# Performance work log

Measured on AMD Instinct MI355X. Metric: run time of the kernel, lower is better.

The kernel has to match this reference:

```python
import jax, jax.numpy as jnp
import numpy as np

B, N_VIS, N_TXT = 2, 2048, 256
N_HEAD, HEAD_DIM = 16, 64
C = N_HEAD * HEAD_DIM  # 1024
EPS = 1e-6


def setup_inputs() -> dict:
    key = jax.random.key(0)
    ks = jax.random.split(key, 24)
    s = 0.02
    inp = {
        'vis_x': jax.random.normal(ks[0], (B, N_VIS, C), jnp.float32),
        'txt_x': jax.random.normal(ks[1], (B, N_TXT, C), jnp.float32),
        'rope_cos': jax.random.uniform(ks[2], (N_VIS, HEAD_DIM), jnp.float32, -1.0, 1.0),
        'rope_sin': jax.random.uniform(ks[3], (N_VIS, HEAD_DIM), jnp.float32, -1.0, 1.0),
    }
    names = ['vis_qw', 'vis_kw', 'vis_vw', 'vis_ow', 'txt_qw', 'txt_kw', 'txt_vw', 'txt_ow']
    for i, n in enumerate(names):
        inp[n] = jax.random.normal(ks[4 + i], (C, C), jnp.float32) * s
        inp[n[:-1] + 'b'] = jnp.zeros((C,), jnp.float32)
    for n in ['vis_qn', 'vis_kn', 'txt_qn', 'txt_kn']:
        inp[n] = jnp.ones((HEAD_DIM,), jnp.float32)
    return inp


def _heads(x, w, b):
    # x: [B,N,C] -> [B,H,N,D]  (torch Linear: x @ W.T + b)
    y = x @ w.T + b
    Bn, N, _ = y.shape
    return y.reshape(Bn, N, N_HEAD, HEAD_DIM).transpose(0, 2, 1, 3)


def _rmsnorm(x, g):
    return x * jax.lax.rsqrt(jnp.mean(x * x, axis=-1, keepdims=True) + EPS) * g


def _rope(x, cos, sin):
    # interleaved-pair rotation: pairs (x0,x1) -> (-x1, x0)
    xr, xi = x[..., 0::2], x[..., 1::2]
    rot = jnp.stack([-xi, xr], axis=-1).reshape(x.shape)
    return x * cos[None, None] + rot * sin[None, None]


def reference(vis_x, txt_x, rope_cos, rope_sin,
              vis_qw, vis_qb, vis_kw, vis_kb, vis_vw, vis_vb, vis_ow, vis_ob,
              txt_qw, txt_qb, txt_kw, txt_kb, txt_vw, txt_vb, txt_ow, txt_ob,
              vis_qn, vis_kn, txt_qn, txt_kn):
    q_vis = _rmsnorm(_heads(vis_x, vis_qw, vis_qb), vis_qn)
    k_vis = _rmsnorm(_heads(vis_x, vis_kw, vis_kb), vis_kn)
    v_vis = _heads(vis_x, vis_vw, vis_vb)
    q_txt = _rmsnorm(_heads(txt_x, txt_qw, txt_qb), txt_qn)
    k_txt = _rmsnorm(_heads(txt_x, txt_kw, txt_kb), txt_kn)
    v_txt = _heads(txt_x, txt_vw, txt_vb)

    q_vis = _rope(q_vis, rope_cos, rope_sin)
    k_vis = _rope(k_vis, rope_cos, rope_sin)

    q = jnp.concatenate([q_txt, q_vis], axis=2)  # [B,H,S,D]
    k = jnp.concatenate([k_txt, k_vis], axis=2)
    v = jnp.concatenate([v_txt, v_vis], axis=2)

    scale = 1.0 / jnp.sqrt(jnp.asarray(HEAD_DIM, q.dtype))
    scores = jnp.einsum('bhqd,bhkd->bhqk', q, k) * scale
    attn = jax.nn.softmax(scores, axis=-1)
    out = jnp.einsum('bhqk,bhkd->bhqd', attn, v)  # [B,H,S,D]

    txt_out = out[:, :, :N_TXT, :].transpose(0, 2, 1, 3).reshape(q.shape[0], N_TXT, C)
    vis_out = out[:, :, N_TXT:, :].transpose(0, 2, 1, 3).reshape(q.shape[0], N_VIS, C)
    vis_out = vis_out @ vis_ow.T + vis_ob
    txt_out = txt_out @ txt_ow.T + txt_ob
    return (vis_out, txt_out)
```

## Files before the change

### kernel.cpp

```cpp
#include <hip/hip_runtime.h>

typedef _Float16 h8 __attribute__((ext_vector_type(8)));
typedef _Float16 h4 __attribute__((ext_vector_type(4)));
typedef _Float16 h2 __attribute__((ext_vector_type(2)));
typedef float f4 __attribute__((ext_vector_type(4)));
typedef float f16x16 __attribute__((ext_vector_type(16)));

#define LOG2E 1.44269504088896340736f

__device__ __forceinline__ void gload_lds16(const void* g, void* l) {
    __builtin_amdgcn_global_load_lds(
        (const __attribute__((address_space(1))) void*)g,
        (__attribute__((address_space(3))) void*)l, 16, 0, 0);
}

struct CastArgs { const float* src[10]; _Float16* dst[10]; };

__global__ __launch_bounds__(256) void cast_all_kernel(CastArgs a) {
    int blk = blockIdx.x;
    int seg, rel;
    if (blk < 4096)      { seg = 0; rel = blk; }
    else if (blk < 4608) { seg = 1; rel = blk - 4096; }
    else { int t = blk - 4608; seg = 2 + (t >> 10); rel = t & 1023; }
    long base = ((long)rel * 256 + threadIdx.x) * 4;
    float4 v = *(const float4*)(a.src[seg] + base);
    h4 o = { (_Float16)v.x, (_Float16)v.y, (_Float16)v.z, (_Float16)v.w };
    *(h4*)(a.dst[seg] + base) = o;
}

struct GemmDesc {
    const _Float16* A[2];
    const _Float16* W[2];
    char*           C[2];
    const float*    bias[2][3];
    long bsA[2];
    long aoff[2];
    long bsC[2];
    int  mshift[2];
    int  mcut;
};

template<bool OUT_F32>
__global__ __launch_bounds__(256)
void gemm_kernel(GemmDesc g, int K, int N, int gm, int gn, int xgn)
{
    __shared__ __align__(16) _Float16 As[128 * 64];
    __shared__ __align__(16) _Float16 Bs[128 * 64];
    const int lane = threadIdx.x & 63;
    const int wave = threadIdx.x >> 6;
    const int lid = blockIdx.x;
    const int xcd = lid & 7;
    const int r0 = lid >> 3;
    const int mtile = (xcd / xgn) * gm + (r0 % gm);
    const int ntile = (xcd % xgn) * gn + (r0 / gm);

    const int seg = mtile >= g.mcut;
    const int mloc = mtile - (seg ? g.mcut : 0);
    const int bidx = mloc >> g.mshift[seg];
    const int min_ = mloc & ((1 << g.mshift[seg]) - 1);
    const _Float16* Ab = g.A[seg] + (long)bidx * g.bsA[seg] + g.aoff[seg]
                         + (long)min_ * 128 * K;
    const _Float16* Bb = g.W[seg] + (long)ntile * 128 * K;
    const long crow0 = (long)bidx * g.bsC[seg] + (long)min_ * 128 * N;

    const int wr = wave >> 1, wc = wave & 1;
    f4 acc[4][4] = {};

    for (int kt = 0; kt < K; kt += 64) {
        __syncthreads();
#pragma unroll
        for (int it = 0; it < 4; ++it) {
            int r = wave * 32 + it * 8 + (lane >> 3);
            int lc = (lane & 7) ^ (r & 7);
            gload_lds16((const char*)(Ab + (long)r * K + kt) + lc * 16,
                        (char*)As + (wave * 32 + it * 8) * 128);
            gload_lds16((const char*)(Bb + (long)r * K + kt) + lc * 16,
                        (char*)Bs + (wave * 32 + it * 8) * 128);
        }
        asm volatile("s_waitcnt vmcnt(0)" ::: "memory");
        __syncthreads();
#pragma unroll
        for (int kk = 0; kk < 2; ++kk) {
            h8 af[4], bf[4];
#pragma unroll
            for (int m = 0; m < 4; ++m) {
                int row = wr * 64 + m * 16 + (lane & 15);
                int pc = (kk * 4 + (lane >> 4)) ^ (row & 7);
                af[m] = *(const h8*)(&As[row * 64 + pc * 8]);
            }
#pragma unroll
            for (int n = 0; n < 4; ++n) {
                int row = wc * 64 + n * 16 + (lane & 15);
                int pc = (kk * 4 + (lane >> 4)) ^ (row & 7);
                bf[n] = *(const h8*)(&Bs[row * 64 + pc * 8]);
            }
#pragma unroll
            for (int m = 0; m < 4; ++m)
#pragma unroll
                for (int n = 0; n < 4; ++n)
                    acc[m][n] = __builtin_amdgcn_mfma_f32_16x16x32_f16(
                        af[m], bf[n], acc[m][n], 0, 0, 0);
        }
    }

#pragma unroll
    for (int n = 0; n < 4; ++n) {
        int col = ntile * 128 + wc * 64 + n * 16 + (lane & 15);
        const float* bp = (col < 1024) ? g.bias[seg][0]
                        : (col < 2048) ? g.bias[seg][1] : g.bias[seg][2];
        float bv = bp[col & 1023];
#pragma unroll
        for (int m = 0; m < 4; ++m) {
            int lrow = wr * 64 + m * 16 + ((lane >> 4) << 2);
#pragma unroll
            for (int r = 0; r < 4; ++r) {
                float v = acc[m][n][r] + bv;
                long off = crow0 + (long)(lrow + r) * N + col;
                if (OUT_F32) ((float*)g.C[seg])[off] = v;
                else         ((_Float16*)g.C[seg])[off] = (_Float16)v;
            }
        }
    }
}

__device__ __forceinline__ float ssum8(h8 v) {
    float s = 0.f;
#pragma unroll
    for (int j = 0; j < 8; ++j) { float f = (float)v[j]; s += f * f; }
    return s;
}
__device__ __forceinline__ float red8(float s) {
    s += __shfl_xor(s, 1); s += __shfl_xor(s, 2); s += __shfl_xor(s, 4);
    return s;
}
__device__ __forceinline__ h8 norm_rope(h8 v, float rs_, const float* g, float gmul,
                                        const float* cs, const float* sn, int vis) {
    float f[8];
#pragma unroll
    for (int j = 0; j < 8; ++j) f[j] = (float)v[j] * rs_ * g[j] * gmul;
    h8 o;
    if (vis) {
#pragma unroll
        for (int j = 0; j < 8; j += 2) {
            float a = f[j], b = f[j + 1];
            o[j]     = (_Float16)(a * cs[j]     - b * sn[j]);
            o[j + 1] = (_Float16)(b * cs[j + 1] + a * sn[j + 1]);
        }
    } else {
#pragma unroll
        for (int j = 0; j < 8; ++j) o[j] = (_Float16)f[j];
    }
    return o;
}

__global__ __launch_bounds__(256)
void pass2_kernel(const _Float16* __restrict__ Yv, const _Float16* __restrict__ Yt,
                  const float* __restrict__ gqv, const float* __restrict__ gkv_,
                  const float* __restrict__ gqt, const float* __restrict__ gkt,
                  const float* __restrict__ rc, const float* __restrict__ rs,
                  _Float16* __restrict__ Q, _Float16* __restrict__ Kd,
                  _Float16* __restrict__ Vt)
{
    const int wave = threadIdx.x >> 6;
    const int lane = threadIdx.x & 63;
    const int row = blockIdx.x * 4 + wave;
    const int is_vis = row < 4096;
    const _Float16* y;
    const float *gq, *gk;
    int b, n, npos;
    if (is_vis) {
        y = Yv + (long)row * 3072; gq = gqv; gk = gkv_;
        b = row >> 11; n = row & 2047; npos = 256 + n;
    } else {
        int r2 = row - 4096;
        y = Yt + (long)r2 * 3072; gq = gqt; gk = gkt;
        b = r2 >> 8; n = r2 & 255; npos = n;
    }
    const int h0 = lane >> 3;
    const int d0 = (lane & 7) * 8;

    h8 q0 = *(const h8*)(y + lane * 8);
    h8 q1 = *(const h8*)(y + 512 + lane * 8);
    h8 k0 = *(const h8*)(y + 1024 + lane * 8);
    h8 k1 = *(const h8*)(y + 1536 + lane * 8);
    h8 v0 = *(const h8*)(y + 2048 + lane * 8);
    h8 v1 = *(const h8*)(y + 2560 + lane * 8);

    float ga[8], gb[8];
    *(float4*)(ga)     = *(const float4*)(gq + d0);
    *(float4*)(ga + 4) = *(const float4*)(gq + d0 + 4);
    *(float4*)(gb)     = *(const float4*)(gk + d0);
    *(float4*)(gb + 4) = *(const float4*)(gk + d0 + 4);
    float cs[8], sn[8];
    if (is_vis) {
        *(float4*)(cs)     = *(const float4*)(rc + n * 64 + d0);
        *(float4*)(cs + 4) = *(const float4*)(rc + n * 64 + d0 + 4);
        *(float4*)(sn)     = *(const float4*)(rs + n * 64 + d0);
        *(float4*)(sn + 4) = *(const float4*)(rs + n * 64 + d0 + 4);
    }

    const float rq0 = rsqrtf(red8(ssum8(q0)) * (1.0f / 64.0f) + 1e-6f);
    const float rq1 = rsqrtf(red8(ssum8(q1)) * (1.0f / 64.0f) + 1e-6f);
    const float rk0 = rsqrtf(red8(ssum8(k0)) * (1.0f / 64.0f) + 1e-6f);
    const float rk1 = rsqrtf(red8(ssum8(k1)) * (1.0f / 64.0f) + 1e-6f);

    const float qmul = 0.125f * LOG2E;
    const long obA = (((long)b * 16 + h0)      * 2304 + npos) * 64 + d0;
    const long obB = (((long)b * 16 + h0 + 8)  * 2304 + npos) * 64 + d0;
    *(h8*)(Q + obA)  = norm_rope(q0, rq0, ga, qmul, cs, sn, is_vis);
    *(h8*)(Q + obB)  = norm_rope(q1, rq1, ga, qmul, cs, sn, is_vis);
    *(h8*)(Kd + obA) = norm_rope(k0, rk0, gb, 1.0f, cs, sn, is_vis);
    *(h8*)(Kd + obB) = norm_rope(k1, rk1, gb, 1.0f, cs, sn, is_vis);

    const long vbA = ((long)(b * 16 + h0)     * 64 + d0) * 2304 + npos;
    const long vbB = ((long)(b * 16 + h0 + 8) * 64 + d0) * 2304 + npos;
#pragma unroll
    for (int j = 0; j < 8; ++j) {
        Vt[vbA + (long)j * 2304] = v0[j];
        Vt[vbB + (long)j * 2304] = v1[j];
    }
}

__device__ __forceinline__ void attn_stage(const char* Kt, const char* Vt, char* S,
                                           int bufB, int t,
                                           int gK0, int gK1, int gV0, int gV1,
                                           int ldsW) {
    const char* kt = Kt + (long)t * 8192;
    const char* vt = Vt + (long)t * 128;
    gload_lds16(kt + gK0, S + bufB + ldsW);
    gload_lds16(kt + gK1, S + bufB + 4096 + ldsW);
    gload_lds16(vt + gV0, S + 16384 + bufB + ldsW);
    gload_lds16(vt + gV1, S + 16384 + bufB + 4096 + ldsW);
}

__device__ __forceinline__ void pv_half(const float* p, const char* S, int vbase,
                                        const int* off, int kblk,
                                        f16x16* oacc, float& psum) {
    const h2 one2 = {(_Float16)1.f, (_Float16)1.f};
#pragma unroll
    for (int kb = 0; kb < 2; ++kb) {
        unsigned w0 = __builtin_bit_cast(unsigned,
            __builtin_amdgcn_cvt_pkrtz(p[8 * kb + 0], p[8 * kb + 1]));
        unsigned w1 = __builtin_bit_cast(unsigned,
            __builtin_amdgcn_cvt_pkrtz(p[8 * kb + 2], p[8 * kb + 3]));
        unsigned w2 = __builtin_bit_cast(unsigned,
            __builtin_amdgcn_cvt_pkrtz(p[8 * kb + 4], p[8 * kb + 5]));
        unsigned w3 = __builtin_bit_cast(unsigned,
            __builtin_amdgcn_cvt_pkrtz(p[8 * kb + 6], p[8 * kb + 7]));
        psum = __builtin_amdgcn_fdot2(__builtin_bit_cast(h2, w0), one2, psum, false);
        psum = __builtin_amdgcn_fdot2(__builtin_bit_cast(h2, w1), one2, psum, false);
        psum = __builtin_amdgcn_fdot2(__builtin_bit_cast(h2, w2), one2, psum, false);
        psum = __builtin_amdgcn_fdot2(__builtin_bit_cast(h2, w3), one2, psum, false);
        asm("v_permlane32_swap_b32 %0, %1" : "+v"(w0), "+v"(w2));
        asm("v_permlane32_swap_b32 %0, %1" : "+v"(w1), "+v"(w3));
        union { unsigned u[4]; h8 v; } pa;
        pa.u[0] = w0; pa.u[1] = w1; pa.u[2] = w2; pa.u[3] = w3;
#pragma unroll
        for (int dblk = 0; dblk < 2; ++dblk) {
            h8 vb = *(const h8*)(S + vbase + dblk * 4096 + off[kblk * 2 + kb]);
            oacc[dblk] = __builtin_amdgcn_mfma_f32_32x32x16_f16(
                pa.v, vb, oacc[dblk], 0, 0, 0);
        }
    }
}

__device__ __forceinline__ void attn_tile(const char* S, int bufB, const int* off,
                                          const h8* qf, f16x16* oacc, float& psum) {
    const f16x16 kZero = {};
    f16x16 st0, st1;
    {
        h8 ka0 = *(const h8*)(S + bufB + off[0]);
        h8 ka1 = *(const h8*)(S + bufB + 4096 + off[0]);
        st0 = __builtin_amdgcn_mfma_f32_32x32x16_f16(ka0, qf[0], kZero, 0, 0, 0);
        st1 = __builtin_amdgcn_mfma_f32_32x32x16_f16(ka1, qf[0], kZero, 0, 0, 0);
    }
#pragma unroll
    for (int ds = 1; ds < 4; ++ds) {
        h8 ka0 = *(const h8*)(S + bufB + off[ds]);
        h8 ka1 = *(const h8*)(S + bufB + 4096 + off[ds]);
        st0 = __builtin_amdgcn_mfma_f32_32x32x16_f16(ka0, qf[ds], st0, 0, 0, 0);
        st1 = __builtin_amdgcn_mfma_f32_32x32x16_f16(ka1, qf[ds], st1, 0, 0, 0);
    }
    float p0[16], p1[16];
#pragma unroll
    for (int r = 0; r < 16; ++r) { p0[r] = exp2f(st0[r]); p1[r] = exp2f(st1[r]); }
    pv_half(p0, S, 16384 + bufB, off, 0, oacc, psum);
    pv_half(p1, S, 16384 + bufB, off, 1, oacc, psum);
}

__global__ __launch_bounds__(256, 4)
void attn_kernel(const _Float16* __restrict__ Qg,
                 const _Float16* __restrict__ Kg,
                 const _Float16* __restrict__ Vg,
                 _Float16* __restrict__ Op,
                 float* __restrict__ Lp,
                 int nt, int cpx)
{
    __shared__ __align__(16) char S[32768];
    const int lane = threadIdx.x & 63;
    const int wave = threadIdx.x >> 6;
    const int l31 = lane & 31, hi = lane >> 5;
    const int d0 = blockIdx.x;
    const int id = (d0 & 7) * cpx + (d0 >> 3);
    const int split = id / 576;
    const int rem = id - split * 576;
    const int bh = rem / 18;
    const int qb = rem - bh * 18;
    const int b = bh >> 4, h = bh & 15;
    const _Float16* Qbh = Qg + (long)bh * 2304 * 64;
    const char* Kt = (const char*)(Kg + (long)bh * 2304 * 64) + (long)split * nt * 8192;
    const char* Vt = (const char*)(Vg + (long)bh * 64 * 2304) + (long)split * nt * 128;
    _Float16* Ops = Op + (long)split * 4718592;
    float* Lps = Lp + (long)split * 73728;
    const int q0 = qb * 128 + wave * 32;

    h8 qf[4];
#pragma unroll
    for (int ds = 0; ds < 4; ++ds)
        qf[ds] = *(const h8*)(Qbh + (long)(q0 + l31) * 64 + ds * 16 + hi * 8);

    const int sg16 = ((lane & 7) ^ (lane >> 3)) * 16;
    const int rK = wave * 8 + (lane >> 3);
    const int gK0 = rK * 128 + sg16;
    const int gK1 = gK0 + 32 * 128;
    const int gV0 = rK * 4608 + sg16;
    const int gV1 = gV0 + 32 * 4608;
    const int ldsW = wave * 1024;
    int off[4];
#pragma unroll
    for (int j = 0; j < 4; ++j)
        off[j] = l31 * 128 + (((j * 2 + hi) ^ (l31 & 7)) * 16);

    f16x16 oacc[2] = {};
    float psum = 0.f;

    attn_stage(Kt, Vt, S, 0, 0, gK0, gK1, gV0, gV1, ldsW);
    asm volatile("s_waitcnt vmcnt(0)" ::: "memory");
    __syncthreads();

    int t = 0;
#pragma unroll 1
    for (int pr = 0; pr < (nt - 1) >> 1; ++pr) {
        attn_stage(Kt, Vt, S, 8192, t + 1, gK0, gK1, gV0, gV1, ldsW);
        __builtin_amdgcn_s_setprio(1);
        attn_tile(S, 0, off, qf, oacc, psum);
        __builtin_amdgcn_s_setprio(0);
        asm volatile("s_waitcnt vmcnt(0)" ::: "memory");
        __syncthreads();
        attn_stage(Kt, Vt, S, 0, t + 2, gK0, gK1, gV0, gV1, ldsW);
        __builtin_amdgcn_s_setprio(1);
        attn_tile(S, 8192, off, qf, oacc, psum);
        __builtin_amdgcn_s_setprio(0);
        asm volatile("s_waitcnt vmcnt(0)" ::: "memory");
        __syncthreads();
        t += 2;
    }
    if (nt & 1) {
        __builtin_amdgcn_s_setprio(1);
        attn_tile(S, 0, off, qf, oacc, psum);
        __builtin_amdgcn_s_setprio(0);
    } else {
        attn_stage(Kt, Vt, S, 8192, nt - 1, gK0, gK1, gV0, gV1, ldsW);
        __builtin_amdgcn_s_setprio(1);
        attn_tile(S, 0, off, qf, oacc, psum);
        __builtin_amdgcn_s_setprio(0);
        asm volatile("s_waitcnt vmcnt(0)" ::: "memory");
        __syncthreads();
        __builtin_amdgcn_s_setprio(1);
        attn_tile(S, 8192, off, qf, oacc, psum);
        __builtin_amdgcn_s_setprio(0);
    }

    float lsum = psum + __shfl_xor(psum, 32);
    if (hi == 0) Lps[(long)bh * 2304 + q0 + l31] = lsum;
#pragma unroll
    for (int dblk = 0; dblk < 2; ++dblk) {
        int dcol = h * 64 + dblk * 32 + l31;
#pragma unroll
        for (int r = 0; r < 16; ++r) {
            int qrow = q0 + (r & 3) + 8 * (r >> 2) + 4 * hi;
            Ops[((long)b * 2304 + qrow) * 1024 + dcol] = (_Float16)oacc[dblk][r];
        }
    }
}

__global__ __launch_bounds__(256)
void combine_kernel(const _Float16* __restrict__ Op,
                    const float* __restrict__ Lp,
                    _Float16* __restrict__ Oh, int ns)
{
    long i = ((long)blockIdx.x * 256 + threadIdx.x) * 8;
    long row = i >> 10;
    int bb = row >= 2304;
    int n = (int)row - bb * 2304;
    int h = ((int)i & 1023) >> 6;
    long lidx = ((long)(bb * 16 + h)) * 2304 + n;
    float l = 0.f;
    float acc[8] = {};
    for (int s = 0; s < ns; ++s) {
        l += Lp[(long)s * 73728 + lidx];
        h8 a = *(const h8*)(Op + (long)s * 4718592 + i);
#pragma unroll
        for (int j = 0; j < 8; ++j) acc[j] += (float)a[j];
    }
    float inv = 1.0f / l;
    h8 o;
#pragma unroll
    for (int j = 0; j < 8; ++j) o[j] = (_Float16)(acc[j] * inv);
    *(h8*)(Oh + i) = o;
}

extern "C" void kernel_launch(void* const* d_in, const int* in_sizes, int n_in,
                              void* d_out, int out_size, void* d_ws, size_t ws_size,
                              hipStream_t stream)
{
    const float* vis_x    = (const float*)d_in[0];
    const float* txt_x    = (const float*)d_in[1];
    const float* rope_cos = (const float*)d_in[2];
    const float* rope_sin = (const float*)d_in[3];
    const float* vis_qw = (const float*)d_in[4];
    const float* vis_qb = (const float*)d_in[5];
    const float* vis_kw = (const float*)d_in[6];
    const float* vis_kb = (const float*)d_in[7];
    const float* vis_vw = (const float*)d_in[8];
    const float* vis_vb = (const float*)d_in[9];
    const float* vis_ow = (const float*)d_in[10];
    const float* vis_ob = (const float*)d_in[11];
    const float* txt_qw = (const float*)d_in[12];
    const float* txt_qb = (const float*)d_in[13];
    const float* txt_kw = (const float*)d_in[14];
    const float* txt_kb = (const float*)d_in[15];
    const float* txt_vw = (const float*)d_in[16];
    const float* txt_vb = (const float*)d_in[17];
    const float* txt_ow = (const float*)d_in[18];
    const float* txt_ob = (const float*)d_in[19];
    const float* vis_qn = (const float*)d_in[20];
    const float* vis_kn = (const float*)d_in[21];
    const float* txt_qn = (const float*)d_in[22];
    const float* txt_kn = (const float*)d_in[23];

    char* ws = (char*)d_ws;
    _Float16* Xvis  = (_Float16*)(ws);
    _Float16* Xtxt  = (_Float16*)(ws + 8388608);
    _Float16* Qh    = (_Float16*)(ws);
    _Float16* WqkvV = (_Float16*)(ws + 9437184);
    _Float16* WqkvT = (_Float16*)(ws + 15728640);
    _Float16* WoV   = (_Float16*)(ws + 22020096);
    _Float16* WoT   = (_Float16*)(ws + 24117248);
    _Float16* Yvis  = (_Float16*)(ws + 26214400);
    _Float16* Ytxt  = (_Float16*)(ws + 51380224);
    _Float16* Kh    = (_Float16*)(ws + 54525952);
    _Float16* Vth   = (_Float16*)(ws + 63963136);

    const int ns = (ws_size >= 112328704) ? 4 : 2;
    const int nt = (ns == 4) ? 9 : 18;
    _Float16* OpP;
    if (ns == 4) OpP = (_Float16*)(ws + 73400320);
    else         OpP = (_Float16*)(ws + 26214400);
    float* LpP = (float*)((char*)OpP + (size_t)ns * 9437184);
    _Float16* Oh = OpP;

    CastArgs ca;
    ca.src[0] = vis_x;  ca.dst[0] = Xvis;
    ca.src[1] = txt_x;  ca.dst[1] = Xtxt;
    ca.src[2] = vis_qw; ca.dst[2] = WqkvV;
    ca.src[3] = vis_kw; ca.dst[3] = WqkvV + 1048576;
    ca.src[4] = vis_vw; ca.dst[4] = WqkvV + 2097152;
    ca.src[5] = txt_qw; ca.dst[5] = WqkvT;
    ca.src[6] = txt_kw; ca.dst[6] = WqkvT + 1048576;
    ca.src[7] = txt_vw; ca.dst[7] = WqkvT + 2097152;
    ca.src[8] = vis_ow; ca.dst[8] = WoV;
    ca.src[9] = txt_ow; ca.dst[9] = WoT;
    cast_all_kernel<<<12800, 256, 0, stream>>>(ca);

    GemmDesc gq;
    gq.A[0] = Xvis;  gq.A[1] = Xtxt;
    gq.W[0] = WqkvV; gq.W[1] = WqkvT;
    gq.C[0] = (char*)Yvis; gq.C[1] = (char*)Ytxt;
    gq.bias[0][0] = vis_qb; gq.bias[0][1] = vis_kb; gq.bias[0][2] = vis_vb;
    gq.bias[1][0] = txt_qb; gq.bias[1][1] = txt_kb; gq.bias[1][2] = txt_vb;
    gq.bsA[0] = 0; gq.bsA[1] = 0;
    gq.aoff[0] = 0; gq.aoff[1] = 0;
    gq.bsC[0] = 0; gq.bsC[1] = 0;
    gq.mshift[0] = 5; gq.mshift[1] = 5;
    gq.mcut = 32;
    gemm_kernel<false><<<864, 256, 0, stream>>>(gq, 1024, 3072, 9, 12, 2);

    pass2_kernel<<<1152, 256, 0, stream>>>(
        Yvis, Ytxt, vis_qn, vis_kn, txt_qn, txt_kn, rope_cos, rope_sin,
        Qh, Kh, Vth);

    attn_kernel<<<576 * ns, 256, 0, stream>>>(Qh, Kh, Vth, OpP, LpP, nt, 72 * ns);
    combine_kernel<<<2304, 256, 0, stream>>>(OpP, LpP, Oh, ns);

    GemmDesc go;
    go.A[0] = Oh; go.A[1] = Oh;
    go.W[0] = WoV; go.W[1] = WoT;
    go.C[0] = (char*)d_out; go.C[1] = (char*)((float*)d_out + 4194304);
    go.bias[0][0] = vis_ob; go.bias[0][1] = vis_ob; go.bias[0][2] = vis_ob;
    go.bias[1][0] = txt_ob; go.bias[1][1] = txt_ob; go.bias[1][2] = txt_ob;
    go.bsA[0] = 2359296;  go.bsA[1] = 2359296;
    go.aoff[0] = 262144;  go.aoff[1] = 0;
    go.bsC[0] = 2097152;  go.bsC[1] = 262144;
    go.mshift[0] = 4; go.mshift[1] = 1;
    go.mcut = 32;
    gemm_kernel<true><<<288, 256, 0, stream>>>(go, 1024, 1024, 9, 4, 2);
}
```

Before: 196.0 us.

## Double-buffer GEMM LDS tiles and restructure attention loop with partial vmcnt waits

The GEMM kernel moves from a single LDS buffer to two, so it prefetches the next K tile with global_load_lds while computing on the current one. It waits with vmcnt(8) so only the older tile's loads have to complete. The attention loop is rewritten as a single ping-pong loop that also waits on only the older stage (vmcnt(4)) and uses raw s_barrier macros in place of __syncthreads. This is meant to overlap global loads with MFMA work and cut barrier stalls, at the cost of twice the GEMM LDS (64KB), which may lower occupancy.

```diff
diff --git a/kernel.cpp b/kernel.cpp
--- a/kernel.cpp
+++ b/kernel.cpp
@@ -7,6 +7,11 @@
 typedef float f16x16 __attribute__((ext_vector_type(16)));
 
 #define LOG2E 1.44269504088896340736f
+
+#define BARRIER_ACQ do { __builtin_amdgcn_s_barrier(); \
+                         asm volatile("" ::: "memory"); } while (0)
+#define BARRIER_REL do { asm volatile("" ::: "memory"); \
+                         __builtin_amdgcn_s_barrier(); } while (0)
 
 __device__ __forceinline__ void gload_lds16(const void* g, void* l) {
     __builtin_amdgcn_global_load_lds(
@@ -44,8 +49,8 @@
 __global__ __launch_bounds__(256)
 void gemm_kernel(GemmDesc g, int K, int N, int gm, int gn, int xgn)
 {
-    __shared__ __align__(16) _Float16 As[128 * 64];
-    __shared__ __align__(16) _Float16 Bs[128 * 64];
+    __shared__ __align__(16) _Float16 As[2][128 * 64];
+    __shared__ __align__(16) _Float16 Bs[2][128 * 64];
     const int lane = threadIdx.x & 63;
     const int wave = threadIdx.x >> 6;
     const int lid = blockIdx.x;
@@ -66,41 +71,54 @@
     const int wr = wave >> 1, wc = wave & 1;
     f4 acc[4][4] = {};
 
-    for (int kt = 0; kt < K; kt += 64) {
-        __syncthreads();
+    auto stage = [&](int bf, int kt) {
 #pragma unroll
         for (int it = 0; it < 4; ++it) {
             int r = wave * 32 + it * 8 + (lane >> 3);
             int lc = (lane & 7) ^ (r & 7);
             gload_lds16((const char*)(Ab + (long)r * K + kt) + lc * 16,
-                        (char*)As + (wave * 32 + it * 8) * 128);
+                        (char*)&As[bf][0] + (wave * 32 + it * 8) * 128);
             gload_lds16((const char*)(Bb + (long)r * K + kt) + lc * 16,
-                        (char*)Bs + (wave * 32 + it * 8) * 128);
-        }
-        asm volatile("s_waitcnt vmcnt(0)" ::: "memory");
-        __syncthreads();
+                        (char*)&Bs[bf][0] + (wave * 32 + it * 8) * 128);
+        }
+    };
+
+    const int nk = K >> 6;
+    stage(0, 0);
+    int buf = 0;
+#pragma unroll 1
+    for (int ki = 0; ki < nk; ++ki) {
+        if (ki + 1 < nk) {
+            stage(buf ^ 1, (ki + 1) << 6);
+            asm volatile("s_waitcnt vmcnt(8)" ::: "memory");
+        } else {
+            asm volatile("s_waitcnt vmcnt(0)" ::: "memory");
+        }
+        BARRIER_ACQ;
 #pragma unroll
         for (int kk = 0; kk < 2; ++kk) {
-            h8 af[4], bf[4];
+            h8 af[4], bf4[4];
 #pragma unroll
             for (int m = 0; m < 4; ++m) {
                 int row = wr * 64 + m * 16 + (lane & 15);
                 int pc = (kk * 4 + (lane >> 4)) ^ (row & 7);
-                af[m] = *(const h8*)(&As[row * 64 + pc * 8]);
+                af[m] = *(const h8*)(&As[buf][row * 64 + pc * 8]);
             }
 #pragma unroll
             for (int n = 0; n < 4; ++n) {
                 int row = wc * 64 + n * 16 + (lane & 15);
                 int pc = (kk * 4 + (lane >> 4)) ^ (row & 7);
-                bf[n] = *(const h8*)(&Bs[row * 64 + pc * 8]);
+                bf4[n] = *(const h8*)(&Bs[buf][row * 64 + pc * 8]);
             }
 #pragma unroll
             for (int m = 0; m < 4; ++m)
 #pragma unroll
                 for (int n = 0; n < 4; ++n)
                     acc[m][n] = __builtin_amdgcn_mfma_f32_16x16x32_f16(
-                        af[m], bf[n], acc[m][n], 0, 0, 0);
-        }
+                        af[m], bf4[n], acc[m][n], 0, 0, 0);
+        }
+        BARRIER_REL;
+        buf ^= 1;
     }
 
 #pragma unroll
@@ -335,40 +353,21 @@
     float psum = 0.f;
 
     attn_stage(Kt, Vt, S, 0, 0, gK0, gK1, gV0, gV1, ldsW);
-    asm volatile("s_waitcnt vmcnt(0)" ::: "memory");
-    __syncthreads();
-
-    int t = 0;
+    int buf = 0;
 #pragma unroll 1
-    for (int pr = 0; pr < (nt - 1) >> 1; ++pr) {
-        attn_stage(Kt, Vt, S, 8192, t + 1, gK0, gK1, gV0, gV1, ldsW);
+    for (int t = 0; t < nt; ++t) {
+        if (t + 1 < nt) {
+            attn_stage(Kt, Vt, S, (buf ^ 1) * 8192, t + 1, gK0, gK1, gV0, gV1, ldsW);
+            asm volatile("s_waitcnt vmcnt(4)" ::: "memory");
+        } else {
+            asm volatile("s_waitcnt vmcnt(0)" ::: "memory");
+        }
+        BARRIER_ACQ;
         __builtin_amdgcn_s_setprio(1);
-        attn_tile(S, 0, off, qf, oacc, psum);
+        attn_tile(S, buf * 8192, off, qf, oacc, psum);
         __builtin_amdgcn_s_setprio(0);
-        asm volatile("s_waitcnt vmcnt(0)" ::: "memory");
-        __syncthreads();
-        attn_stage(Kt, Vt, S, 0, t + 2, gK0, gK1, gV0, gV1, ldsW);
-        __builtin_amdgcn_s_setprio(1);
-        attn_tile(S, 8192, off, qf, oacc, psum);
-        __builtin_amdgcn_s_setprio(0);
-        asm volatile("s_waitcnt vmcnt(0)" ::: "memory");
-        __syncthreads();
-        t += 2;
-    }
-    if (nt & 1) {
-        __builtin_amdgcn_s_setprio(1);
-        attn_tile(S, 0, off, qf, oacc, psum);
-        __builtin_amdgcn_s_setprio(0);
-    } else {
-        attn_stage(Kt, Vt, S, 8192, nt - 1, gK0, gK1, gV0, gV1, ldsW);
-        __builtin_amdgcn_s_setprio(1);
-        attn_tile(S, 0, off, qf, oacc, psum);
-        __builtin_amdgcn_s_setprio(0);
-        asm volatile("s_waitcnt vmcnt(0)" ::: "memory");
-        __syncthreads();
-        __builtin_amdgcn_s_setprio(1);
-        attn_tile(S, 8192, off, qf, oacc, psum);
-        __builtin_amdgcn_s_setprio(0);
+        BARRIER_REL;
+        buf ^= 1;
     }
 
     float lsum = psum + __shfl_xor(psum, 32);
```

New measurement: 192.7 us. Within noise of the previous version (-1.7%).
